# Performance work log

Hardware: AMD Instinct MI355X
Metric: run time of the kernel (lower is better)

## Reference

```python
import jax, jax.numpy as jnp
import numpy as np

B, S, D, E, H, TOPK = 4, 2048, 1024, 32, 128, 4

def setup_inputs() -> dict:
    key = jax.random.key(0)
    k1, k2, k3, k4 = jax.random.split(key, 4)
    x = jax.random.normal(k1, (B, S, D), jnp.float32)
    expert_sel = jax.random.normal(k2, (E, D), jnp.float32) * (D ** -0.5)
    keys = jax.random.normal(k3, (E, D, H), jnp.float32) * (D ** -0.5)
    values = jax.random.normal(k4, (E, H, D), jnp.float32) * (H ** -0.5)
    return {"x": x, "expert_sel": expert_sel, "keys": keys, "values": values, "n_heads": TOPK}

def reference(x, expert_sel, keys, values, n_heads):
    # x: [B,S,D]; expert_sel: [E,D]; keys: [E,D,H]; values: [E,H,D]
    Bv, Sv, Dv = x.shape
    Ev = keys.shape[0]
    xf = x.reshape(-1, Dv)                                  # [N,D]
    N = xf.shape[0]
    gate = jax.nn.sigmoid(xf @ expert_sel.T)                # [N,E] sigmoid gating (sigma-MoE)
    vals, idx = jax.lax.top_k(gate, n_heads)                # [N,k] selected experts + gate weights
    # dense per-token-per-expert gate weights; zero for non-selected experts
    g = jnp.zeros((N, Ev), x.dtype).at[jnp.arange(N)[:, None], idx].set(vals)  # [N,E]
    # grouped expert FFN, expressed densely over the (small) expert axis:
    # out = sum_e g[n,e] * relu(x @ keys[e]) @ values[e]
    h = jax.nn.relu(jnp.einsum('nd,edh->enh', xf, keys))    # [E,N,H]
    out = jnp.einsum('enh,ehd->nd', h * g.T[:, :, None], values)  # [N,D]
    return out.reshape(Bv, Sv, Dv)
```

## Files before the change

kernel.cpp:

```cpp
#include <hip/hip_runtime.h>
#include <hip/hip_bf16.h>

#define NTOK 8192
#define DDIM 1024
#define NEXP 32
#define HDIM 128
#define TOPK 4

typedef __attribute__((ext_vector_type(8))) short bf16x8;
typedef __attribute__((ext_vector_type(4))) float f32x4;

typedef unsigned int uint_g __attribute__((address_space(1)));
typedef unsigned int uint_l __attribute__((address_space(3)));

__device__ __forceinline__ void async_cp16(const void* g, void* l) {
    __builtin_amdgcn_global_load_lds((const uint_g*)g, (uint_l*)l, 16, 0, 0);
}

__device__ inline unsigned short f2bf(float f) {
    unsigned int u = __builtin_bit_cast(unsigned int, f);
    unsigned int r = (u + 0x7fffu + ((u >> 16) & 1u)) >> 16;
    return (unsigned short)r;
}
__device__ inline float bf2f(unsigned short s) {
    unsigned int u = ((unsigned int)s) << 16;
    return __builtin_bit_cast(float, u);
}

__global__ __launch_bounds__(256) void prep_gate(
    const float* __restrict__ x, const float* __restrict__ es,
    const float* __restrict__ keys, const float* __restrict__ values,
    unsigned short* __restrict__ Kb, unsigned short* __restrict__ Vb,
    unsigned short* __restrict__ Xb,
    int* __restrict__ cnt, int* __restrict__ tok_list, float* __restrict__ gates)
{
    const int tid = threadIdx.x;

    if (blockIdx.x < 4096) {
        int idx = blockIdx.x * 256 + tid;
        unsigned short o[8];
        if (idx < NEXP * 128 * 128) {
            int n = idx & 127, k0 = (idx >> 7) & 127, e = idx >> 14;
            const float* s = keys + ((size_t)e * DDIM + k0 * 8) * HDIM + n;
            #pragma unroll
            for (int j = 0; j < 8; ++j) o[j] = f2bf(s[(size_t)j * HDIM]);
            *(uint4*)&Kb[(size_t)idx * 8] = *(uint4*)o;
        } else {
            idx -= NEXP * 128 * 128;
            int n = idx & 1023, k0 = (idx >> 10) & 15, e = idx >> 14;
            const float* s = values + ((size_t)e * HDIM + k0 * 8) * DDIM + n;
            #pragma unroll
            for (int j = 0; j < 8; ++j) o[j] = f2bf(s[(size_t)j * DDIM]);
            *(uint4*)&Vb[(size_t)idx * 8] = *(uint4*)o;
        }
        return;
    }

    const int n0 = (int)(blockIdx.x - 4096) * 16;

    __shared__ float smem[4608];
    __shared__ float Ls[16 * 33];
    __shared__ int hist[NEXP];
    __shared__ int bbase[NEXP];
    float* Xt  = smem;
    float* Est = smem + 64 * 36;
    float* Lp  = smem;

    const int t4  = (tid & 3) * 4;
    const int e4  = ((tid >> 2) & 7) * 4;
    const int rep = tid >> 5;

    const int xr = tid & 15, xc4 = (tid >> 4) * 4;
    const int er = tid & 31, ec8 = (tid >> 5) * 8;

    const int ctok = tid >> 4, cd4 = (tid & 15) * 4;

    const int rtok = tid >> 5, re = tid & 31;

    float lsum[2] = {0.f, 0.f};

    if (tid < NEXP) hist[tid] = 0;

    for (int q = 0; q < 4; ++q) {
        float acc[4][4] = {};

        for (int dc = q * 256; dc < q * 256 + 256; dc += 64) {
            __syncthreads();
            {
                float4 v = *(const float4*)&x[(size_t)(n0 + xr) * DDIM + dc + xc4];
                Xt[(xc4 + 0) * 36 + xr] = v.x; Xt[(xc4 + 1) * 36 + xr] = v.y;
                Xt[(xc4 + 2) * 36 + xr] = v.z; Xt[(xc4 + 3) * 36 + xr] = v.w;
            }
            #pragma unroll
            for (int i = 0; i < 2; ++i) {
                float4 v = *(const float4*)&es[(size_t)er * DDIM + dc + ec8 + i * 4];
                Est[(ec8 + i * 4 + 0) * 36 + er] = v.x;
                Est[(ec8 + i * 4 + 1) * 36 + er] = v.y;
                Est[(ec8 + i * 4 + 2) * 36 + er] = v.z;
                Est[(ec8 + i * 4 + 3) * 36 + er] = v.w;
            }
            __syncthreads();

            {
                unsigned short o[4];
                #pragma unroll
                for (int j = 0; j < 4; ++j) o[j] = f2bf(Xt[(cd4 + j) * 36 + ctok]);
                *(uint2*)&Xb[(size_t)(n0 + ctok) * DDIM + dc + cd4] = *(uint2*)o;
            }

            #pragma unroll
            for (int s = 0; s < 8; ++s) {
                int d = s * 8 + rep;
                float4 xv = *(const float4*)&Xt[d * 36 + t4];
                float4 ev = *(const float4*)&Est[d * 36 + e4];
                const float xa[4] = {xv.x, xv.y, xv.z, xv.w};
                const float ea[4] = {ev.x, ev.y, ev.z, ev.w};
                #pragma unroll
                for (int i = 0; i < 4; ++i)
                    #pragma unroll
                    for (int j = 0; j < 4; ++j)
                        acc[i][j] = fmaf(xa[i], ea[j], acc[i][j]);
            }
        }

        __syncthreads();
        #pragma unroll
        for (int i = 0; i < 4; ++i)
            #pragma unroll
            for (int j = 0; j < 4; ++j)
                Lp[(rep * 16 + t4 + i) * 33 + e4 + j] = acc[i][j];
        __syncthreads();

        #pragma unroll
        for (int h = 0; h < 2; ++h) {
            int tok = rtok + h * 8;
            float s = 0.f;
            #pragma unroll
            for (int r = 0; r < 8; ++r) s += Lp[(r * 16 + tok) * 33 + re];
            lsum[h] += s;
        }
    }

    #pragma unroll
    for (int h = 0; h < 2; ++h) Ls[(rtok + h * 8) * 33 + re] = lsum[h];
    __syncthreads();

    int sel[TOPK]; int lpos[TOPK];
    if (tid < 16) {
        float lg[NEXP];
        #pragma unroll
        for (int e2 = 0; e2 < NEXP; ++e2) lg[e2] = Ls[tid * 33 + e2];
        float sv[TOPK];
        #pragma unroll
        for (int j = 0; j < TOPK; ++j) {
            float bv = -3.0e38f; int bi = 0;
            #pragma unroll
            for (int e2 = 0; e2 < NEXP; ++e2) {
                bool taken = false;
                #pragma unroll
                for (int q = 0; q < j; ++q) taken = taken || (sel[q] == e2);
                float v = taken ? -3.0e38f : lg[e2];
                if (v > bv) { bv = v; bi = e2; }
            }
            sel[j] = bi; sv[j] = bv;
        }
        #pragma unroll
        for (int j = 0; j < TOPK; ++j) {
            gates[(size_t)(n0 + tid) * TOPK + j] = 1.f / (1.f + expf(-sv[j]));
            lpos[j] = atomicAdd(&hist[sel[j]], 1);
        }
    }
    __syncthreads();
    if (tid < NEXP) bbase[tid] = atomicAdd(&cnt[tid], hist[tid]);
    __syncthreads();
    if (tid < 16) {
        #pragma unroll
        for (int j = 0; j < TOPK; ++j)
            tok_list[(size_t)sel[j] * NTOK + bbase[sel[j]] + lpos[j]] = (n0 + tid) * TOPK + j;
    }
}

__global__ __launch_bounds__(256) void ffn_fused(
    const unsigned short* __restrict__ Xb,
    const unsigned short* __restrict__ Kb,
    const unsigned short* __restrict__ Vb,
    const int* __restrict__ cnt, const int* __restrict__ tok_list,
    const float* __restrict__ gates,
    unsigned short* __restrict__ Ob)
{
    const int bid = blockIdx.x;
    const int e = bid & 31, tile = bid >> 5;
    const int c = cnt[e], base = tile * 64;
    if (base >= c) return;
    const int nt   = min(64, c - base);
    const int tid  = threadIdx.x, wave = tid >> 6, lane = tid & 63;
    const int lm   = lane & 15, quad = lane >> 4;
    const int r2   = (wave >> 1) * 32;
    const int c2   = (wave & 1) * 64;
    const int cw   = (wave & 1) * 32;

    __shared__ __align__(16) unsigned short KV[8192];
    __shared__ __align__(16) unsigned short XO[4608];
    __shared__ __align__(16) unsigned short Hs[64 * 140];
    __shared__ int slot[64]; __shared__ int gtok[64]; __shared__ float gs[64];

    if (tid < 64) {
        if (tid < nt) {
            int v = tok_list[(size_t)e * NTOK + base + tid];
            slot[tid] = v; gtok[tid] = v >> 2; gs[tid] = gates[v];
        } else { slot[tid] = -1; gtok[tid] = 0; gs[tid] = 0.f; }
    }
    __syncthreads();

    const unsigned short* Ke    = Kb + (size_t)e * 131072;
    const unsigned short* Ve    = Vb + (size_t)e * 131072;
    const unsigned short* xrowb = Xb + (size_t)gtok[lane] * DDIM;

    f32x4 acc[2][4];
    #pragma unroll
    for (int i = 0; i < 2; ++i)
        #pragma unroll
        for (int j = 0; j < 4; ++j) acc[i][j] = (f32x4){0.f, 0.f, 0.f, 0.f};

    auto stageA = [&](int t) {
        int dc = t * 64;
        #pragma unroll
        for (int i = 0; i < 4; ++i) {
            int p = wave * 4 + i;
            async_cp16(Ke + ((size_t)(dc / 8 + (p >> 1)) * 128 + (p & 1) * 64 + lane) * 8,
                       &KV[p * 512]);
        }
        #pragma unroll
        for (int i = 0; i < 2; ++i) {
            int k0 = wave * 2 + i;
            async_cp16(xrowb + dc + k0 * 8, &XO[k0 * 512]);
        }
    };

    stageA(0);
    __syncthreads();

    for (int t = 0; t < 16; ++t) {
        #pragma unroll
        for (int ks = 0; ks < 2; ++ks) {
            int k0 = ks * 4 + quad;
            bf16x8 a0 = *(const bf16x8*)&XO[(k0 * 64 + r2 + lm) * 8];
            bf16x8 a1 = *(const bf16x8*)&XO[(k0 * 64 + r2 + 16 + lm) * 8];
            #pragma unroll
            for (int tj = 0; tj < 4; ++tj) {
                bf16x8 bb = *(const bf16x8*)&KV[(k0 * 128 + c2 + tj * 16 + lm) * 8];
                acc[0][tj] = __builtin_amdgcn_mfma_f32_16x16x32_bf16(a0, bb, acc[0][tj], 0, 0, 0);
                acc[1][tj] = __builtin_amdgcn_mfma_f32_16x16x32_bf16(a1, bb, acc[1][tj], 0, 0, 0);
            }
        }
        if (t < 15) {
            __syncthreads();
            stageA(t + 1);
            __syncthreads();
        }
    }

    #pragma unroll
    for (int ti = 0; ti < 2; ++ti)
        #pragma unroll
        for (int reg = 0; reg < 4; ++reg) {
            int m = r2 + ti * 16 + quad * 4 + reg;
            float g = gs[m];
            #pragma unroll
            for (int tj = 0; tj < 4; ++tj)
                Hs[m * 140 + c2 + tj * 16 + lm] = f2bf(fmaxf(acc[ti][tj][reg], 0.f) * g);
        }
    __syncthreads();

    auto stageV = [&](int cc) {
        #pragma unroll
        for (int i = 0; i < 4; ++i) {
            int p = wave * 4 + i;
            async_cp16(Ve + ((size_t)p * 1024 + cc * 64 + lane) * 8, &KV[p * 512]);
        }
    };

    stageV(0);
    __syncthreads();

    const int om = tid >> 2, oq = tid & 3;
    const int os = slot[om];

    for (int cc = 0; cc < 16; ++cc) {
        f32x4 acc2[2][2];
        #pragma unroll
        for (int i = 0; i < 2; ++i) {
            acc2[i][0] = (f32x4){0.f, 0.f, 0.f, 0.f};
            acc2[i][1] = (f32x4){0.f, 0.f, 0.f, 0.f};
        }

        #pragma unroll
        for (int ks = 0; ks < 4; ++ks) {
            int k0 = ks * 4 + quad;
            bf16x8 a0 = *(const bf16x8*)&Hs[(r2 + lm) * 140 + k0 * 8];
            bf16x8 a1 = *(const bf16x8*)&Hs[(r2 + 16 + lm) * 140 + k0 * 8];
            #pragma unroll
            for (int tj = 0; tj < 2; ++tj) {
                bf16x8 bb = *(const bf16x8*)&KV[(k0 * 64 + cw + tj * 16 + lm) * 8];
                acc2[0][tj] = __builtin_amdgcn_mfma_f32_16x16x32_bf16(a0, bb, acc2[0][tj], 0, 0, 0);
                acc2[1][tj] = __builtin_amdgcn_mfma_f32_16x16x32_bf16(a1, bb, acc2[1][tj], 0, 0, 0);
            }
        }

        #pragma unroll
        for (int ti = 0; ti < 2; ++ti)
            #pragma unroll
            for (int reg = 0; reg < 4; ++reg) {
                int m = r2 + ti * 16 + quad * 4 + reg;
                XO[m * 72 + cw + lm]      = f2bf(acc2[ti][0][reg]);
                XO[m * 72 + cw + 16 + lm] = f2bf(acc2[ti][1][reg]);
            }
        __syncthreads();

        if (os >= 0) {
            uint4 v0 = *(const uint4*)&XO[om * 72 + oq * 16];
            uint4 v1 = *(const uint4*)&XO[om * 72 + oq * 16 + 8];
            unsigned short* op = Ob + (size_t)os * DDIM + cc * 64 + oq * 16;
            *(uint4*)op       = v0;
            *(uint4*)(op + 8) = v1;
        }
        if (cc < 15) stageV(cc + 1);
        __syncthreads();
    }
}

__global__ __launch_bounds__(256) void reduce_out(
    const unsigned short* __restrict__ Ob, float* __restrict__ out)
{
    const int tid = threadIdx.x;
    const int n   = blockIdx.x * 2 + (tid >> 7);
    const int cc  = (tid & 127) * 8;

    float s[8] = {};
    #pragma unroll
    for (int j = 0; j < 4; ++j) {
        uint4 v = *(const uint4*)&Ob[((size_t)n * 4 + j) * DDIM + cc];
        const unsigned int w[4] = {v.x, v.y, v.z, v.w};
        #pragma unroll
        for (int q = 0; q < 4; ++q) {
            s[q * 2 + 0] += bf2f((unsigned short)(w[q] & 0xffff));
            s[q * 2 + 1] += bf2f((unsigned short)(w[q] >> 16));
        }
    }
    float4 o0 = {s[0], s[1], s[2], s[3]};
    float4 o1 = {s[4], s[5], s[6], s[7]};
    *(float4*)&out[(size_t)n * DDIM + cc]     = o0;
    *(float4*)&out[(size_t)n * DDIM + cc + 4] = o1;
}

extern "C" void kernel_launch(void* const* d_in, const int* in_sizes, int n_in,
                              void* d_out, int out_size, void* d_ws, size_t ws_size,
                              hipStream_t stream) {
    const float* x      = (const float*)d_in[0];
    const float* es     = (const float*)d_in[1];
    const float* keys   = (const float*)d_in[2];
    const float* values = (const float*)d_in[3];
    float* out          = (float*)d_out;

    char* w = (char*)d_ws;
    int*   cnt      = (int*)w;               w += 256;
    int*   tok_list = (int*)w;               w += (size_t)NEXP * NTOK * sizeof(int);
    float* gates    = (float*)w;             w += (size_t)NTOK * TOPK * sizeof(float);
    unsigned short* Kb = (unsigned short*)w; w += (size_t)NEXP * 128 * 128 * 8 * 2;
    unsigned short* Vb = (unsigned short*)w; w += (size_t)NEXP * 16 * 1024 * 8 * 2;
    unsigned short* Xb = (unsigned short*)w; w += (size_t)NTOK * DDIM * 2;
    unsigned short* Ob = (unsigned short*)w;

    hipMemsetAsync(cnt, 0, NEXP * sizeof(int), stream);

    prep_gate<<<4096 + NTOK / 16, 256, 0, stream>>>(x, es, keys, values, Kb, Vb, Xb,
                                                    cnt, tok_list, gates);
    ffn_fused<<<128 * NEXP, 256, 0, stream>>>(Xb, Kb, Vb, cnt, tok_list, gates, Ob);
    reduce_out<<<NTOK / 2, 256, 0, stream>>>(Ob, out);
}
```

Before: 213.3 us.

## Reorder prep blocks, prefetch gate loads, swizzle X staging, hoist H fragments

Result: faster. 186.3 us (-12.7%).

```diff
diff --git a/kernel.cpp b/kernel.cpp
--- a/kernel.cpp
+++ b/kernel.cpp
@@ -36,8 +36,8 @@
 {
     const int tid = threadIdx.x;
 
-    if (blockIdx.x < 4096) {
-        int idx = blockIdx.x * 256 + tid;
+    if (blockIdx.x >= 512) {
+        int idx = (int)(blockIdx.x - 512) * 256 + tid;
         unsigned short o[8];
         if (idx < NEXP * 128 * 128) {
             int n = idx & 127, k0 = (idx >> 7) & 127, e = idx >> 14;
@@ -56,7 +56,7 @@
         return;
     }
 
-    const int n0 = (int)(blockIdx.x - 4096) * 16;
+    const int n0 = (int)blockIdx.x * 16;
 
     __shared__ float smem[4608];
     __shared__ float Ls[16 * 33];
@@ -81,23 +81,29 @@
 
     if (tid < NEXP) hist[tid] = 0;
 
+    float4 xv  = *(const float4*)&x[(size_t)(n0 + xr) * DDIM + xc4];
+    float4 ev0 = *(const float4*)&es[(size_t)er * DDIM + ec8];
+    float4 ev1 = *(const float4*)&es[(size_t)er * DDIM + ec8 + 4];
+
     for (int q = 0; q < 4; ++q) {
         float acc[4][4] = {};
 
-        for (int dc = q * 256; dc < q * 256 + 256; dc += 64) {
+        for (int dci = 0; dci < 4; ++dci) {
+            const int dc = q * 256 + dci * 64;
             __syncthreads();
             {
-                float4 v = *(const float4*)&x[(size_t)(n0 + xr) * DDIM + dc + xc4];
-                Xt[(xc4 + 0) * 36 + xr] = v.x; Xt[(xc4 + 1) * 36 + xr] = v.y;
-                Xt[(xc4 + 2) * 36 + xr] = v.z; Xt[(xc4 + 3) * 36 + xr] = v.w;
-            }
-            #pragma unroll
-            for (int i = 0; i < 2; ++i) {
-                float4 v = *(const float4*)&es[(size_t)er * DDIM + dc + ec8 + i * 4];
-                Est[(ec8 + i * 4 + 0) * 36 + er] = v.x;
-                Est[(ec8 + i * 4 + 1) * 36 + er] = v.y;
-                Est[(ec8 + i * 4 + 2) * 36 + er] = v.z;
-                Est[(ec8 + i * 4 + 3) * 36 + er] = v.w;
+                Xt[(xc4 + 0) * 36 + xr] = xv.x; Xt[(xc4 + 1) * 36 + xr] = xv.y;
+                Xt[(xc4 + 2) * 36 + xr] = xv.z; Xt[(xc4 + 3) * 36 + xr] = xv.w;
+                Est[(ec8 + 0) * 36 + er] = ev0.x; Est[(ec8 + 1) * 36 + er] = ev0.y;
+                Est[(ec8 + 2) * 36 + er] = ev0.z; Est[(ec8 + 3) * 36 + er] = ev0.w;
+                Est[(ec8 + 4) * 36 + er] = ev1.x; Est[(ec8 + 5) * 36 + er] = ev1.y;
+                Est[(ec8 + 6) * 36 + er] = ev1.z; Est[(ec8 + 7) * 36 + er] = ev1.w;
+            }
+            const int nxt = dc + 64;
+            if (nxt < DDIM) {
+                xv  = *(const float4*)&x[(size_t)(n0 + xr) * DDIM + nxt + xc4];
+                ev0 = *(const float4*)&es[(size_t)er * DDIM + nxt + ec8];
+                ev1 = *(const float4*)&es[(size_t)er * DDIM + nxt + ec8 + 4];
             }
             __syncthreads();
 
@@ -111,10 +117,10 @@
             #pragma unroll
             for (int s = 0; s < 8; ++s) {
                 int d = s * 8 + rep;
-                float4 xv = *(const float4*)&Xt[d * 36 + t4];
-                float4 ev = *(const float4*)&Est[d * 36 + e4];
-                const float xa[4] = {xv.x, xv.y, xv.z, xv.w};
-                const float ea[4] = {ev.x, ev.y, ev.z, ev.w};
+                float4 xa4 = *(const float4*)&Xt[d * 36 + t4];
+                float4 ea4 = *(const float4*)&Est[d * 36 + e4];
+                const float xa[4] = {xa4.x, xa4.y, xa4.z, xa4.w};
+                const float ea[4] = {ea4.x, ea4.y, ea4.z, ea4.w};
                 #pragma unroll
                 for (int i = 0; i < 4; ++i)
                     #pragma unroll
@@ -158,7 +164,7 @@
             for (int e2 = 0; e2 < NEXP; ++e2) {
                 bool taken = false;
                 #pragma unroll
-                for (int q = 0; q < j; ++q) taken = taken || (sel[q] == e2);
+                for (int qq = 0; qq < j; ++qq) taken = taken || (sel[qq] == e2);
                 float v = taken ? -3.0e38f : lg[e2];
                 if (v > bv) { bv = v; bi = e2; }
             }
@@ -212,9 +218,8 @@
     }
     __syncthreads();
 
-    const unsigned short* Ke    = Kb + (size_t)e * 131072;
-    const unsigned short* Ve    = Vb + (size_t)e * 131072;
-    const unsigned short* xrowb = Xb + (size_t)gtok[lane] * DDIM;
+    const unsigned short* Ke = Kb + (size_t)e * 131072;
+    const unsigned short* Ve = Vb + (size_t)e * 131072;
 
     f32x4 acc[2][4];
     #pragma unroll
@@ -222,6 +227,8 @@
         #pragma unroll
         for (int j = 0; j < 4; ++j) acc[i][j] = (f32x4){0.f, 0.f, 0.f, 0.f};
 
+    const int xrow = (lane >> 3);
+    const int xsub = (lane & 7);
     auto stageA = [&](int t) {
         int dc = t * 64;
         #pragma unroll
@@ -232,20 +239,24 @@
         }
         #pragma unroll
         for (int i = 0; i < 2; ++i) {
-            int k0 = wave * 2 + i;
-            async_cp16(xrowb + dc + k0 * 8, &XO[k0 * 512]);
+            int j = wave * 2 + i;
+            int row = j * 8 + xrow;
+            int u = xsub ^ (row & 7);
+            async_cp16(Xb + (size_t)gtok[row] * DDIM + dc + u * 8, &XO[j * 512]);
         }
     };
 
     stageA(0);
     __syncthreads();
 
+    const int xx = (quad << 3);
     for (int t = 0; t < 16; ++t) {
         #pragma unroll
         for (int ks = 0; ks < 2; ++ks) {
             int k0 = ks * 4 + quad;
-            bf16x8 a0 = *(const bf16x8*)&XO[(k0 * 64 + r2 + lm) * 8];
-            bf16x8 a1 = *(const bf16x8*)&XO[(k0 * 64 + r2 + 16 + lm) * 8];
+            int xo = ((k0 ^ (lm & 7)) & 7) * 8;
+            bf16x8 a0 = *(const bf16x8*)&XO[(r2 + lm) * 64 + xo];
+            bf16x8 a1 = *(const bf16x8*)&XO[(r2 + 16 + lm) * 64 + xo];
             #pragma unroll
             for (int tj = 0; tj < 4; ++tj) {
                 bf16x8 bb = *(const bf16x8*)&KV[(k0 * 128 + c2 + tj * 16 + lm) * 8];
@@ -259,6 +270,7 @@
             __syncthreads();
         }
     }
+    (void)xx;
 
     #pragma unroll
     for (int ti = 0; ti < 2; ++ti)
@@ -281,6 +293,13 @@
     };
 
     stageV(0);
+
+    bf16x8 hf[2][4];
+    #pragma unroll
+    for (int ks = 0; ks < 4; ++ks) {
+        hf[0][ks] = *(const bf16x8*)&Hs[(r2 + lm) * 140 + (ks * 4 + quad) * 8];
+        hf[1][ks] = *(const bf16x8*)&Hs[(r2 + 16 + lm) * 140 + (ks * 4 + quad) * 8];
+    }
     __syncthreads();
 
     const int om = tid >> 2, oq = tid & 3;
@@ -297,13 +316,11 @@
         #pragma unroll
         for (int ks = 0; ks < 4; ++ks) {
             int k0 = ks * 4 + quad;
-            bf16x8 a0 = *(const bf16x8*)&Hs[(r2 + lm) * 140 + k0 * 8];
-            bf16x8 a1 = *(const bf16x8*)&Hs[(r2 + 16 + lm) * 140 + k0 * 8];
             #pragma unroll
             for (int tj = 0; tj < 2; ++tj) {
                 bf16x8 bb = *(const bf16x8*)&KV[(k0 * 64 + cw + tj * 16 + lm) * 8];
-                acc2[0][tj] = __builtin_amdgcn_mfma_f32_16x16x32_bf16(a0, bb, acc2[0][tj], 0, 0, 0);
-                acc2[1][tj] = __builtin_amdgcn_mfma_f32_16x16x32_bf16(a1, bb, acc2[1][tj], 0, 0, 0);
+                acc2[0][tj] = __builtin_amdgcn_mfma_f32_16x16x32_bf16(hf[0][ks], bb, acc2[0][tj], 0, 0, 0);
+                acc2[1][tj] = __builtin_amdgcn_mfma_f32_16x16x32_bf16(hf[1][ks], bb, acc2[1][tj], 0, 0, 0);
             }
         }
 
@@ -373,8 +390,8 @@
 
     hipMemsetAsync(cnt, 0, NEXP * sizeof(int), stream);
 
-    prep_gate<<<4096 + NTOK / 16, 256, 0, stream>>>(x, es, keys, values, Kb, Vb, Xb,
-                                                    cnt, tok_list, gates);
+    prep_gate<<<512 + 4096, 256, 0, stream>>>(x, es, keys, values, Kb, Vb, Xb,
+                                              cnt, tok_list, gates);
     ffn_fused<<<128 * NEXP, 256, 0, stream>>>(Xb, Kb, Vb, cnt, tok_list, gates, Ob);
     reduce_out<<<NTOK / 2, 256, 0, stream>>>(Ob, out);
 }
```
